# Optimization experiments

Measured on AMD Instinct MI355X. Metric: run time of the kernel, lower is better.

The kernel has to match this reference:

```python
import jax, jax.numpy as jnp
import numpy as np

B, N, E, F_IN, F_OUT = 4, 50000, 800000, 128, 128


def setup_inputs() -> dict:
    key = jax.random.key(0)
    k1, k2, k3, k4, k5 = jax.random.split(key, 5)
    x = jax.random.normal(k1, (B, N, F_IN), dtype=jnp.float32)
    # nn.Linear(in, out, bias=False) weight: [out_features, in_features]
    W = jax.random.normal(k2, (F_OUT, F_IN), dtype=jnp.float32) * (1.0 / np.sqrt(F_IN))
    edge_row = jax.random.randint(k3, (E,), 0, N, dtype=jnp.int64)
    edge_col = jax.random.randint(k4, (E,), 0, N, dtype=jnp.int64)
    edge_vals = jax.random.uniform(k5, (E,), dtype=jnp.float32)
    return {"x": x, "W": W, "edge_row": edge_row, "edge_col": edge_col, "edge_vals": edge_vals}


def reference(x, W, edge_row, edge_col, edge_vals):
    # x: [B, N, F_in]; linear projection (no bias): h = x @ W^T -> [B, N, F_out]
    h = jnp.einsum('bnf,of->bno', x, W)

    # SpMM: out[r] = sum_{edges (r,c)} A[r,c] * h[c], vmapped over batch
    def spmm(hb):  # hb: [N, F_out]
        msg = hb[edge_col] * edge_vals[:, None]  # [E, F_out]
        return jax.ops.segment_sum(msg, edge_row, num_segments=N)

    return jax.vmap(spmm)(h)  # [B, N, F_out]
```

## Files before the change

kernel.cpp:

```cpp
#include <hip/hip_runtime.h>
#include <stdint.h>

#define NB 4
#define NN 50000
#define NE 800000
#define NF 128

#define NBLK 49
#define LDK 72

typedef __attribute__((ext_vector_type(8))) short  bfrag;
typedef __attribute__((ext_vector_type(4))) float  ffrag;
typedef __attribute__((ext_vector_type(4))) short  short4v;

__device__ inline unsigned short f2bf(float f) {
    unsigned int u = __builtin_bit_cast(unsigned int, f);
    u += 0x7fffu + ((u >> 16) & 1u);
    return (unsigned short)(u >> 16);
}
__device__ inline float bflo(unsigned int u) { return __builtin_bit_cast(float, u << 16); }
__device__ inline float bfhi(unsigned int u) { return __builtin_bit_cast(float, u & 0xffff0000u); }

__global__ __launch_bounds__(256) void gemm_kernel(
    const float* __restrict__ x,
    const float* __restrict__ W,
    unsigned short* __restrict__ h,
    int M)
{
    __shared__ short xs[128 * LDK];
    __shared__ short wsh[128 * LDK];

    const int tid  = threadIdx.x;
    const int w    = tid >> 6;
    const int lane = tid & 63;
    const int wr   = w >> 1;
    const int wc   = w & 1;
    const int q    = lane >> 4;
    const int l15  = lane & 15;
    const int m0   = blockIdx.x * 128;

    ffrag acc[4][4];
#pragma unroll
    for (int i = 0; i < 4; ++i)
#pragma unroll
        for (int j = 0; j < 4; ++j) acc[i][j] = (ffrag)0.f;

    for (int kc = 0; kc < 2; ++kc) {
        const int c = kc * 64;
        __syncthreads();
#pragma unroll
        for (int it = 0; it < 8; ++it) {
            int linear = it * 256 + tid;
            int r  = linear >> 4;
            int k4 = linear & 15;

            float4 wv = *(const float4*)(W + (size_t)r * NF + c + k4 * 4);
            short4v wsv;
            wsv[0] = (short)f2bf(wv.x); wsv[1] = (short)f2bf(wv.y);
            wsv[2] = (short)f2bf(wv.z); wsv[3] = (short)f2bf(wv.w);
            *(short4v*)&wsh[r * LDK + k4 * 4] = wsv;

            int gr = m0 + r;
            float4 xv = make_float4(0.f, 0.f, 0.f, 0.f);
            if (gr < M) xv = *(const float4*)(x + (size_t)gr * NF + c + k4 * 4);
            short4v xsv;
            xsv[0] = (short)f2bf(xv.x); xsv[1] = (short)f2bf(xv.y);
            xsv[2] = (short)f2bf(xv.z); xsv[3] = (short)f2bf(xv.w);
            *(short4v*)&xs[r * LDK + k4 * 4] = xsv;
        }
        __syncthreads();

#pragma unroll
        for (int ks = 0; ks < 2; ++ks) {
            const int ko = ks * 32 + q * 8;
            bfrag a[4], b[4];
#pragma unroll
            for (int i = 0; i < 4; ++i)
                a[i] = *(const bfrag*)&xs[(wr * 64 + i * 16 + l15) * LDK + ko];
#pragma unroll
            for (int j = 0; j < 4; ++j)
                b[j] = *(const bfrag*)&wsh[(wc * 64 + j * 16 + l15) * LDK + ko];
#pragma unroll
            for (int i = 0; i < 4; ++i)
#pragma unroll
                for (int j = 0; j < 4; ++j)
                    acc[i][j] = __builtin_amdgcn_mfma_f32_16x16x32_bf16(
                        a[i], b[j], acc[i][j], 0, 0, 0);
        }
    }

#pragma unroll
    for (int i = 0; i < 4; ++i) {
#pragma unroll
        for (int reg = 0; reg < 4; ++reg) {
            int m = m0 + wr * 64 + i * 16 + q * 4 + reg;
            if (m < M) {
                int n  = m % NN;
                int bb = m / NN;
                unsigned short* hp = h + ((size_t)n * NB + bb) * NF;
#pragma unroll
                for (int j = 0; j < 4; ++j) {
                    int col = wc * 64 + j * 16 + l15;
                    hp[col] = f2bf(acc[i][j][reg]);
                }
            }
        }
    }
}

__global__ void hist_kernel(const int* __restrict__ row, int* __restrict__ cnt)
{
    int e = blockIdx.x * 256 + threadIdx.x;
    if (e < NE) atomicAdd(&cnt[row[e]], 1);
}

__global__ __launch_bounds__(1024) void scan1_kernel(
    const int* __restrict__ cnt, int* __restrict__ rs, int* __restrict__ bsum)
{
    __shared__ int wsum[16];
    const int tid  = threadIdx.x;
    const int lane = tid & 63;
    const int wid  = tid >> 6;
    const int i    = blockIdx.x * 1024 + tid;

    int v = (i < NN) ? cnt[i] : 0;
    int incl = v;
#pragma unroll
    for (int off = 1; off < 64; off <<= 1) {
        int t = __shfl_up(incl, off, 64);
        if (lane >= off) incl += t;
    }
    if (lane == 63) wsum[wid] = incl;
    __syncthreads();
    int woff = 0;
    for (int ww = 0; ww < wid; ++ww) woff += wsum[ww];
    if (i < NN) rs[i] = woff + incl - v;
    if (tid == 0) {
        int tot = 0;
        for (int ww = 0; ww < 16; ++ww) tot += wsum[ww];
        bsum[blockIdx.x] = tot;
    }
}

__global__ void scan2_kernel(int* __restrict__ bsum, int* __restrict__ rs)
{
    int lane = threadIdx.x;
    int v = (lane < NBLK) ? bsum[lane] : 0;
    int incl = v;
#pragma unroll
    for (int off = 1; off < 64; off <<= 1) {
        int t = __shfl_up(incl, off, 64);
        if (lane >= off) incl += t;
    }
    if (lane < NBLK) bsum[lane] = incl - v;
    if (lane == 63) rs[NN] = incl;
}

__global__ __launch_bounds__(1024) void scan3_kernel(
    int* __restrict__ rs, const int* __restrict__ bsum, int* __restrict__ cursor)
{
    int i = blockIdx.x * 1024 + threadIdx.x;
    if (i < NN) {
        rs[i] += bsum[blockIdx.x];
        cursor[i] = 0;
    }
}

__global__ void scatter_kernel(const int* __restrict__ row,
                               const int* __restrict__ col,
                               const float* __restrict__ val,
                               const int* __restrict__ rs,
                               int* __restrict__ cursor,
                               uint2* __restrict__ cv_s)
{
    int e = blockIdx.x * 256 + threadIdx.x;
    if (e < NE) {
        int r   = row[e];
        int p   = atomicAdd(&cursor[r], 1);
        int dst = rs[r] + p;
        uint2 cv;
        cv.x = (unsigned)col[e];
        cv.y = __builtin_bit_cast(unsigned, val[e]);
        cv_s[dst] = cv;
    }
}

__global__ __launch_bounds__(256) void spmm_kernel(
    const unsigned short* __restrict__ h,
    const int* __restrict__ rs,
    const uint2* __restrict__ cv_s,
    float* __restrict__ out)
{
    const int w    = threadIdx.x >> 6;
    const int lane = threadIdx.x & 63;
    const int r    = blockIdx.x * 4 + w;
    if (r >= NN) return;

    const int s = rs[r];
    const int e = rs[r + 1];
    const int b  = lane >> 4;
    const int f0 = (lane & 15) * 8;
    const size_t lane_off = (size_t)b * NF + f0;

    float acc[8];
#pragma unroll
    for (int k = 0; k < 8; ++k) acc[k] = 0.f;

    int i = s;
    for (; i + 4 <= e; i += 4) {
        uint2 cv0 = cv_s[i];
        uint2 cv1 = cv_s[i + 1];
        uint2 cv2 = cv_s[i + 2];
        uint2 cv3 = cv_s[i + 3];
        const uint4 q0 = *(const uint4*)(h + (size_t)cv0.x * (NB * NF) + lane_off);
        const uint4 q1 = *(const uint4*)(h + (size_t)cv1.x * (NB * NF) + lane_off);
        const uint4 q2 = *(const uint4*)(h + (size_t)cv2.x * (NB * NF) + lane_off);
        const uint4 q3 = *(const uint4*)(h + (size_t)cv3.x * (NB * NF) + lane_off);
        float v0 = __builtin_bit_cast(float, cv0.y);
        float v1 = __builtin_bit_cast(float, cv1.y);
        float v2 = __builtin_bit_cast(float, cv2.y);
        float v3 = __builtin_bit_cast(float, cv3.y);
        acc[0] += v0 * bflo(q0.x); acc[1] += v0 * bfhi(q0.x);
        acc[2] += v0 * bflo(q0.y); acc[3] += v0 * bfhi(q0.y);
        acc[4] += v0 * bflo(q0.z); acc[5] += v0 * bfhi(q0.z);
        acc[6] += v0 * bflo(q0.w); acc[7] += v0 * bfhi(q0.w);
        acc[0] += v1 * bflo(q1.x); acc[1] += v1 * bfhi(q1.x);
        acc[2] += v1 * bflo(q1.y); acc[3] += v1 * bfhi(q1.y);
        acc[4] += v1 * bflo(q1.z); acc[5] += v1 * bfhi(q1.z);
        acc[6] += v1 * bflo(q1.w); acc[7] += v1 * bfhi(q1.w);
        acc[0] += v2 * bflo(q2.x); acc[1] += v2 * bfhi(q2.x);
        acc[2] += v2 * bflo(q2.y); acc[3] += v2 * bfhi(q2.y);
        acc[4] += v2 * bflo(q2.z); acc[5] += v2 * bfhi(q2.z);
        acc[6] += v2 * bflo(q2.w); acc[7] += v2 * bfhi(q2.w);
        acc[0] += v3 * bflo(q3.x); acc[1] += v3 * bfhi(q3.x);
        acc[2] += v3 * bflo(q3.y); acc[3] += v3 * bfhi(q3.y);
        acc[4] += v3 * bflo(q3.z); acc[5] += v3 * bfhi(q3.z);
        acc[6] += v3 * bflo(q3.w); acc[7] += v3 * bfhi(q3.w);
    }
    for (; i < e; ++i) {
        uint2 cv = cv_s[i];
        float v  = __builtin_bit_cast(float, cv.y);
        const uint4 qv = *(const uint4*)(h + (size_t)cv.x * (NB * NF) + lane_off);
        acc[0] += v * bflo(qv.x); acc[1] += v * bfhi(qv.x);
        acc[2] += v * bflo(qv.y); acc[3] += v * bfhi(qv.y);
        acc[4] += v * bflo(qv.z); acc[5] += v * bfhi(qv.z);
        acc[6] += v * bflo(qv.w); acc[7] += v * bfhi(qv.w);
    }

    float* op = out + ((size_t)b * NN + r) * NF + f0;
    *(float4*)op       = make_float4(acc[0], acc[1], acc[2], acc[3]);
    *(float4*)(op + 4) = make_float4(acc[4], acc[5], acc[6], acc[7]);
}

extern "C" void kernel_launch(void* const* d_in, const int* in_sizes, int n_in,
                              void* d_out, int out_size, void* d_ws, size_t ws_size,
                              hipStream_t stream)
{
    const float* x    = (const float*)d_in[0];
    const float* W    = (const float*)d_in[1];
    const int*   erow = (const int*)d_in[2];
    const int*   ecol = (const int*)d_in[3];
    const float* ev   = (const float*)d_in[4];
    float*       out  = (float*)d_out;

    char*  ws  = (char*)d_ws;
    size_t off = 0;
    auto alloc = [&](size_t bytes) -> void* {
        void* p = ws + off;
        off += (bytes + 255) & ~(size_t)255;
        return p;
    };
    unsigned short* h = (unsigned short*)alloc((size_t)NN * NB * NF * sizeof(unsigned short));
    int*   rs     = (int*)  alloc((size_t)(NN + 1) * sizeof(int));
    int*   cnt    = (int*)  alloc((size_t)NN * sizeof(int));
    int*   cursor = (int*)  alloc((size_t)NN * sizeof(int));
    int*   bsum   = (int*)  alloc((size_t)64 * sizeof(int));
    uint2* cv_s   = (uint2*)alloc((size_t)NE * sizeof(uint2));

    hipMemsetAsync(cnt, 0, (size_t)NN * sizeof(int), stream);

    const int M = NB * NN;
    gemm_kernel<<<(M + 127) / 128, 256, 0, stream>>>(x, W, h, M);

    hist_kernel<<<(NE + 255) / 256, 256, 0, stream>>>(erow, cnt);
    scan1_kernel<<<NBLK, 1024, 0, stream>>>(cnt, rs, bsum);
    scan2_kernel<<<1, 64, 0, stream>>>(bsum, rs);
    scan3_kernel<<<NBLK, 1024, 0, stream>>>(rs, bsum, cursor);
    scatter_kernel<<<(NE + 255) / 256, 256, 0, stream>>>(erow, ecol, ev, rs,
                                                         cursor, cv_s);

    spmm_kernel<<<(NN + 3) / 4, 256, 0, stream>>>(h, rs, cv_s, out);
}
```

Measured before the change: 422.4 us.

## Fuse histogram into GEMM, stage GEMM output through LDS, drop scan3 pass

Moves the per-row edge histogram into the GEMM kernel as a grid-stride prologue, which removes a separate launch. The bf16 GEMM epilogue now writes the output tile to shared memory first and then stores it with coalesced 16-byte writes, replacing scattered 2-byte stores. The scan3 kernel is removed: the block offset is added lazily in scatter and spmm via bsum[r>>10], and a single memset now zeroes both cnt and cursor. The cost is extra atomic work inside the GEMM and one more index lookup on the consumer side.

```diff
diff --git a/kernel.cpp b/kernel.cpp
--- a/kernel.cpp
+++ b/kernel.cpp
@@ -8,6 +8,7 @@
 
 #define NBLK 49
 #define LDK 72
+#define LDT 136
 
 typedef __attribute__((ext_vector_type(8))) short  bfrag;
 typedef __attribute__((ext_vector_type(4))) float  ffrag;
@@ -25,12 +26,19 @@
     const float* __restrict__ x,
     const float* __restrict__ W,
     unsigned short* __restrict__ h,
+    const int* __restrict__ erow,
+    int* __restrict__ cnt,
     int M)
 {
-    __shared__ short xs[128 * LDK];
-    __shared__ short wsh[128 * LDK];
+    __shared__ short smem[2 * 128 * LDK];
+    short* xs  = smem;
+    short* wsh = smem + 128 * LDK;
 
     const int tid  = threadIdx.x;
+
+    for (int e = blockIdx.x * 256 + tid; e < NE; e += gridDim.x * 256)
+        atomicAdd(&cnt[erow[e]], 1);
+
     const int w    = tid >> 6;
     const int lane = tid & 63;
     const int wr   = w >> 1;
@@ -89,29 +97,30 @@
         }
     }
 
-#pragma unroll
-    for (int i = 0; i < 4; ++i) {
+    __syncthreads();
+    short* tile = smem;
+#pragma unroll
+    for (int i = 0; i < 4; ++i)
 #pragma unroll
         for (int reg = 0; reg < 4; ++reg) {
-            int m = m0 + wr * 64 + i * 16 + q * 4 + reg;
-            if (m < M) {
-                int n  = m % NN;
-                int bb = m / NN;
-                unsigned short* hp = h + ((size_t)n * NB + bb) * NF;
-#pragma unroll
-                for (int j = 0; j < 4; ++j) {
-                    int col = wc * 64 + j * 16 + l15;
-                    hp[col] = f2bf(acc[i][j][reg]);
-                }
-            }
-        }
-    }
-}
-
-__global__ void hist_kernel(const int* __restrict__ row, int* __restrict__ cnt)
-{
-    int e = blockIdx.x * 256 + threadIdx.x;
-    if (e < NE) atomicAdd(&cnt[row[e]], 1);
+            int row = wr * 64 + i * 16 + q * 4 + reg;
+#pragma unroll
+            for (int j = 0; j < 4; ++j)
+                tile[row * LDT + wc * 64 + j * 16 + l15] =
+                    (short)f2bf(acc[i][j][reg]);
+        }
+    __syncthreads();
+#pragma unroll
+    for (int it = 0; it < 8; ++it) {
+        int row = it * 16 + (tid >> 4);
+        int m   = m0 + row;
+        if (m < M) {
+            int n  = m % NN;
+            int bb = m / NN;
+            uint4 v = *(const uint4*)&tile[row * LDT + (tid & 15) * 8];
+            *(uint4*)(h + ((size_t)n * NB + bb) * NF + (tid & 15) * 8) = v;
+        }
+    }
 }
 
 __global__ __launch_bounds__(1024) void scan1_kernel(
@@ -142,7 +151,7 @@
     }
 }
 
-__global__ void scan2_kernel(int* __restrict__ bsum, int* __restrict__ rs)
+__global__ void scan2_kernel(int* __restrict__ bsum)
 {
     int lane = threadIdx.x;
     int v = (lane < NBLK) ? bsum[lane] : 0;
@@ -153,23 +162,13 @@
         if (lane >= off) incl += t;
     }
     if (lane < NBLK) bsum[lane] = incl - v;
-    if (lane == 63) rs[NN] = incl;
-}
-
-__global__ __launch_bounds__(1024) void scan3_kernel(
-    int* __restrict__ rs, const int* __restrict__ bsum, int* __restrict__ cursor)
-{
-    int i = blockIdx.x * 1024 + threadIdx.x;
-    if (i < NN) {
-        rs[i] += bsum[blockIdx.x];
-        cursor[i] = 0;
-    }
 }
 
 __global__ void scatter_kernel(const int* __restrict__ row,
                                const int* __restrict__ col,
                                const float* __restrict__ val,
                                const int* __restrict__ rs,
+                               const int* __restrict__ bsum,
                                int* __restrict__ cursor,
                                uint2* __restrict__ cv_s)
 {
@@ -177,7 +176,7 @@
     if (e < NE) {
         int r   = row[e];
         int p   = atomicAdd(&cursor[r], 1);
-        int dst = rs[r] + p;
+        int dst = rs[r] + bsum[r >> 10] + p;
         uint2 cv;
         cv.x = (unsigned)col[e];
         cv.y = __builtin_bit_cast(unsigned, val[e]);
@@ -188,6 +187,7 @@
 __global__ __launch_bounds__(256) void spmm_kernel(
     const unsigned short* __restrict__ h,
     const int* __restrict__ rs,
+    const int* __restrict__ bsum,
     const uint2* __restrict__ cv_s,
     float* __restrict__ out)
 {
@@ -196,8 +196,8 @@
     const int r    = blockIdx.x * 4 + w;
     if (r >= NN) return;
 
-    const int s = rs[r];
-    const int e = rs[r + 1];
+    const int s = rs[r] + bsum[r >> 10];
+    const int e = (r + 1 == NN) ? NE : rs[r + 1] + bsum[(r + 1) >> 10];
     const int b  = lane >> 4;
     const int f0 = (lane & 15) * 8;
     const size_t lane_off = (size_t)b * NF + f0;
@@ -272,22 +272,20 @@
     };
     unsigned short* h = (unsigned short*)alloc((size_t)NN * NB * NF * sizeof(unsigned short));
     int*   rs     = (int*)  alloc((size_t)(NN + 1) * sizeof(int));
-    int*   cnt    = (int*)  alloc((size_t)NN * sizeof(int));
-    int*   cursor = (int*)  alloc((size_t)NN * sizeof(int));
+    int*   cnt    = (int*)  alloc((size_t)2 * NN * sizeof(int));
+    int*   cursor = cnt + NN;
     int*   bsum   = (int*)  alloc((size_t)64 * sizeof(int));
     uint2* cv_s   = (uint2*)alloc((size_t)NE * sizeof(uint2));
 
-    hipMemsetAsync(cnt, 0, (size_t)NN * sizeof(int), stream);
+    hipMemsetAsync(cnt, 0, (size_t)2 * NN * sizeof(int), stream);
 
     const int M = NB * NN;
-    gemm_kernel<<<(M + 127) / 128, 256, 0, stream>>>(x, W, h, M);
-
-    hist_kernel<<<(NE + 255) / 256, 256, 0, stream>>>(erow, cnt);
+    gemm_kernel<<<(M + 127) / 128, 256, 0, stream>>>(x, W, h, erow, cnt, M);
+
     scan1_kernel<<<NBLK, 1024, 0, stream>>>(cnt, rs, bsum);
-    scan2_kernel<<<1, 64, 0, stream>>>(bsum, rs);
-    scan3_kernel<<<NBLK, 1024, 0, stream>>>(rs, bsum, cursor);
+    scan2_kernel<<<1, 64, 0, stream>>>(bsum);
     scatter_kernel<<<(NE + 255) / 256, 256, 0, stream>>>(erow, ecol, ev, rs,
-                                                         cursor, cv_s);
-
-    spmm_kernel<<<(NN + 3) / 4, 256, 0, stream>>>(h, rs, cv_s, out);
-}
+                                                         bsum, cursor, cv_s);
+
+    spmm_kernel<<<(NN + 3) / 4, 256, 0, stream>>>(h, rs, bsum, cv_s, out);
+}
```

New measurement: 406.0 us. -3.9%, faster.
